# Kernel tuning notes

Measured on AMD Instinct MI355X. Metric: run time of the kernel, lower is better.

## Reference

```python
import jax, jax.numpy as jnp
import numpy as np

B, T, N, O = 128, 256, 64, 32
E, H = 32, 64            # embed_dim, hyper_dim
S = O * 4 + 1            # state_dim = 129


def setup_inputs() -> dict:
    key = jax.random.key(0)
    ks = jax.random.split(key, 16)
    def lin(k, i, o):
        return jax.random.normal(k, (i, o), jnp.float32) * (1.0 / np.sqrt(i))
    inp = {}
    inp["agent_qs"] = jax.random.normal(ks[0], (B, T, N), jnp.float32)
    inp["obs"] = jax.random.normal(ks[1], (B, T, N, O), jnp.float32)
    inp["agent_mask"] = jax.random.randint(ks[2], (B, N), 0, 2).astype(jnp.int32)
    # hyper_w_1: Linear(S,H) -> ReLU -> Linear(H, N*E)
    inp["w1_1"] = lin(ks[3], S, H); inp["b1_1"] = jnp.zeros((H,), jnp.float32)
    inp["w1_2"] = lin(ks[4], H, N * E); inp["b1_2"] = jnp.zeros((N * E,), jnp.float32)
    # hyper_w_2: Linear(S,H) -> ReLU -> Linear(H, E)
    inp["w2_1"] = lin(ks[5], S, H); inp["b2_1"] = jnp.zeros((H,), jnp.float32)
    inp["w2_2"] = lin(ks[6], H, E); inp["b2_2"] = jnp.zeros((E,), jnp.float32)
    # hyper_b_1: Linear(S,E)
    inp["wb1"] = lin(ks[7], S, E); inp["bb1"] = jnp.zeros((E,), jnp.float32)
    # hyper_b_2: Linear(S,E) -> ReLU -> Linear(E,1)
    inp["wb2_1"] = lin(ks[8], S, E); inp["bb2_1"] = jnp.zeros((E,), jnp.float32)
    inp["wb2_2"] = lin(ks[9], E, 1); inp["bb2_2"] = jnp.zeros((1,), jnp.float32)
    return inp


def _state_features(obs, agent_mask):
    # Faithful to torch loop: stats over the FIRST k agents where k = mask.sum().
    b, t, n, o = obs.shape
    k = agent_mask.sum(axis=1)                                   # [B]
    am = (jnp.arange(n)[None, :] < k[:, None]).astype(obs.dtype)  # [B,N]
    m = am[:, None, :, None]                                      # [B,1,N,1]
    cnt = k.astype(obs.dtype)[:, None, None]                      # [B,1,1]
    safe = jnp.maximum(cnt, 1.0)
    mean = (obs * m).sum(axis=2) / safe                           # [B,T,O]
    var = (((obs - mean[:, :, None, :]) ** 2) * m).sum(axis=2) / jnp.maximum(cnt - 1.0, 1.0)
    std = jnp.where(cnt > 1.0, jnp.sqrt(var), 0.0)                # unbiased std, 0 if k<=1
    mb = m > 0
    mn = jnp.where(mb, obs, jnp.inf).min(axis=2)
    mx = jnp.where(mb, obs, -jnp.inf).max(axis=2)
    ratio = jnp.broadcast_to(cnt / n, (b, t, 1))
    feats = jnp.concatenate([mean, std, mn, mx, ratio], axis=-1)  # [B,T,S]
    return jnp.where(cnt > 0.0, feats, 0.0)                       # rows stay zero if k==0


def reference(agent_qs, obs, agent_mask,
              w1_1, b1_1, w1_2, b1_2,
              w2_1, b2_1, w2_2, b2_2,
              wb1, bb1, wb2_1, bb2_1, wb2_2, bb2_2):
    b, t, n = agent_qs.shape
    e = wb1.shape[1]
    states = _state_features(obs, agent_mask)                     # [B,T,S]
    s = states.reshape(b * t, -1)                                 # [BT,S]
    qs = agent_qs.reshape(b * t, n)                               # [BT,N]
    w1 = jnp.abs(jax.nn.relu(s @ w1_1 + b1_1) @ w1_2 + b1_2).reshape(b * t, n, e)
    b1 = s @ wb1 + bb1                                            # [BT,E]
    hidden = jax.nn.elu(jnp.einsum('bn,bne->be', qs, w1) + b1)    # [BT,E]
    w2 = jnp.abs(jax.nn.relu(s @ w2_1 + b2_1) @ w2_2 + b2_2)      # [BT,E]
    b2 = jax.nn.relu(s @ wb2_1 + bb2_1) @ wb2_2 + bb2_2           # [BT,1]
    q_tot = (hidden * w2).sum(axis=-1, keepdims=True) + b2        # [BT,1]
    return q_tot.reshape(b, t, 1)
```

## Files before the change

kernel.cpp:

```cpp
#include <hip/hip_runtime.h>
#include <math.h>

#define BB 128
#define TT 256
#define NN 64
#define OO 32
#define EE 32
#define HH 64
#define SS 129
#define BT 32768
#define SP 132

__global__ __launch_bounds__(256) void k_states(const float* __restrict__ obs,
                                                const int* __restrict__ mask,
                                                float* __restrict__ states) {
    int w = threadIdx.x >> 6;
    int l = threadIdx.x & 63;
    int bt = blockIdx.x * 4 + w;
    int b = bt >> 8;

    int kv = mask[(b << 6) + l];
    #pragma unroll
    for (int off = 32; off; off >>= 1) kv += __shfl_xor(kv, off);

    int o = l & 31, nh = l >> 5;
    float sum = 0.f, ssq = 0.f, mn = INFINITY, mx = -INFINITY;
    const float* op = obs + ((size_t)bt << 11);
    for (int n = nh; n < kv; n += 2) {
        float v = op[(n << 5) + o];
        sum += v;
        ssq = fmaf(v, v, ssq);
        mn = fminf(mn, v);
        mx = fmaxf(mx, v);
    }
    sum += __shfl_xor(sum, 32);
    ssq += __shfl_xor(ssq, 32);
    mn = fminf(mn, __shfl_xor(mn, 32));
    mx = fmaxf(mx, __shfl_xor(mx, 32));

    float kf = (float)kv;
    float mean = sum / fmaxf(kf, 1.f);
    float var = (ssq - kf * mean * mean) / fmaxf(kf - 1.f, 1.f);
    float sd = (kv > 1) ? sqrtf(fmaxf(var, 0.f)) : 0.f;
    if (kv == 0) { mean = 0.f; sd = 0.f; mn = 0.f; mx = 0.f; }

    float* sp = states + (size_t)bt * SP;
    if (l < 32) {
        sp[o] = mean;
        sp[32 + o] = sd;
        sp[64 + o] = mn;
        sp[96 + o] = mx;
    }
    if (l == 0) {
        sp[128] = kf * 0.015625f;
        sp[129] = 0.f; sp[130] = 0.f; sp[131] = 0.f;
    }
}

__global__ __launch_bounds__(256, 3) void k_mlp1(const float* __restrict__ states,
        const float* __restrict__ w1_1, const float* __restrict__ b1_1,
        const float* __restrict__ w2_1, const float* __restrict__ b2_1,
        const float* __restrict__ wb1,  const float* __restrict__ bb1,
        const float* __restrict__ wb2_1,const float* __restrict__ bb2_1,
        float* __restrict__ h1, float* __restrict__ t2,
        float* __restrict__ b1v, float* __restrict__ t3) {
    __shared__ float wl[SP * 96];
    __shared__ float bl[96];
    int t = threadIdx.x;
    int half = blockIdx.y;

    const float* wA = half ? w2_1 : w1_1;
    const float* wB = half ? wb2_1 : wb1;
    const float* bA = half ? b2_1 : b1_1;
    const float* bB = half ? bb2_1 : bb1;
    float* outA = half ? t2 : h1;
    float* outB = half ? t3 : b1v;
    int reluB = half;

    for (int idx = t; idx < SP * 96; idx += 256) {
        int k = idx / 96;
        int c = idx - k * 96;
        float v = 0.f;
        if (k < SS) v = (c < 64) ? wA[k * 64 + c] : wB[k * 32 + (c - 64)];
        wl[idx] = v;
    }
    if (t < 96) bl[t] = (t < 64) ? bA[t] : bB[t - 64];
    __syncthreads();

    int cg = t & 7, rg = t >> 3;
    int c0 = cg * 12;
    int row0 = blockIdx.x * 128 + rg * 4;
    float acc[4][12];
    #pragma unroll
    for (int i = 0; i < 4; i++)
        #pragma unroll
        for (int j = 0; j < 12; j++) acc[i][j] = 0.f;

    const float* s0 = states + (size_t)row0 * SP;
    for (int k0 = 0; k0 < SP; k0 += 4) {
        float sv[4][4];
        #pragma unroll
        for (int i = 0; i < 4; i++)
            *(float4*)&sv[i][0] = *(const float4*)(s0 + i * SP + k0);
        #pragma unroll
        for (int kk = 0; kk < 4; kk++) {
            float wv[12];
            #pragma unroll
            for (int q = 0; q < 3; q++)
                *(float4*)&wv[q * 4] = *(const float4*)&wl[(k0 + kk) * 96 + c0 + q * 4];
            #pragma unroll
            for (int i = 0; i < 4; i++) {
                float s = sv[i][kk];
                #pragma unroll
                for (int j = 0; j < 12; j++) acc[i][j] = fmaf(s, wv[j], acc[i][j]);
            }
        }
    }

    #pragma unroll
    for (int i = 0; i < 4; i++) {
        int row = row0 + i;
        #pragma unroll
        for (int j = 0; j < 12; j++) {
            int c = c0 + j;
            float v = acc[i][j] + bl[c];
            if (c < 64) {
                v = fmaxf(v, 0.f);
                outA[(size_t)row * 64 + c] = v;
            } else {
                if (reluB) v = fmaxf(v, 0.f);
                outB[(size_t)row * 32 + (c - 64)] = v;
            }
        }
    }
}

__global__ __launch_bounds__(256) void k_w2(const float* __restrict__ t2,
        const float* __restrict__ t3, const float* __restrict__ w2_2,
        const float* __restrict__ b2_2, const float* __restrict__ wb2_2,
        const float* __restrict__ bb2_2,
        float* __restrict__ w2, float* __restrict__ b2v) {
    __shared__ float wl[64 * 32];
    __shared__ float wb[32];
    __shared__ float bb[32];
    int t = threadIdx.x;
    for (int idx = t; idx < 2048; idx += 256) wl[idx] = w2_2[idx];
    if (t < 32) wb[t] = wb2_2[t];
    if (t >= 32 && t < 64) bb[t - 32] = b2_2[t - 32];
    __syncthreads();

    int r = t >> 2, eq = t & 3;
    int row = blockIdx.x * 64 + r;
    int e0 = eq * 8;
    float acc[8];
    #pragma unroll
    for (int j = 0; j < 8; j++) acc[j] = 0.f;

    const float* tp = t2 + (size_t)row * 64;
    for (int h4 = 0; h4 < 64; h4 += 4) {
        float tv[4];
        *(float4*)tv = *(const float4*)(tp + h4);
        #pragma unroll
        for (int hh = 0; hh < 4; hh++) {
            float s = tv[hh];
            float4 wv0 = *(const float4*)&wl[(h4 + hh) * 32 + e0];
            float4 wv1 = *(const float4*)&wl[(h4 + hh) * 32 + e0 + 4];
            acc[0] = fmaf(s, wv0.x, acc[0]); acc[1] = fmaf(s, wv0.y, acc[1]);
            acc[2] = fmaf(s, wv0.z, acc[2]); acc[3] = fmaf(s, wv0.w, acc[3]);
            acc[4] = fmaf(s, wv1.x, acc[4]); acc[5] = fmaf(s, wv1.y, acc[5]);
            acc[6] = fmaf(s, wv1.z, acc[6]); acc[7] = fmaf(s, wv1.w, acc[7]);
        }
    }
    #pragma unroll
    for (int j = 0; j < 8; j++)
        w2[(size_t)row * 32 + e0 + j] = fabsf(acc[j] + bb[e0 + j]);

    if (eq == 0) {
        const float* t3p = t3 + (size_t)row * 32;
        float a = 0.f;
        #pragma unroll
        for (int q = 0; q < 8; q++) {
            float4 v3 = *(const float4*)(t3p + q * 4);
            float4 wv = *(const float4*)&wb[q * 4];
            a = fmaf(v3.x, wv.x, a); a = fmaf(v3.y, wv.y, a);
            a = fmaf(v3.z, wv.z, a); a = fmaf(v3.w, wv.w, a);
        }
        b2v[row] = a + bb2_2[0];
    }
}

__global__ __launch_bounds__(256, 4) void k_main(
        const float* __restrict__ h1g, const float* __restrict__ qsg,
        const float* __restrict__ w12, const float* __restrict__ b12,
        const float* __restrict__ b1vg, const float* __restrict__ w2g,
        const float* __restrict__ b2vg, float* __restrict__ out) {
    __shared__ float h1T[64 * 64];
    __shared__ float Wp[64 * 64];
    __shared__ float hid[64 * 32];
    int t = threadIdx.x;
    int row0 = blockIdx.x * 64;

    {
        int r = t >> 2, h0 = (t & 3) * 16;
        const float* hp = h1g + (size_t)(row0 + r) * 64 + h0;
        #pragma unroll
        for (int q = 0; q < 4; q++) {
            float4 hv = *(const float4*)(hp + q * 4);
            int hb = h0 + q * 4;
            h1T[(hb + 0) * 64 + r] = hv.x;
            h1T[(hb + 1) * 64 + r] = hv.y;
            h1T[(hb + 2) * 64 + r] = hv.z;
            h1T[(hb + 3) * 64 + r] = hv.w;
        }
    }

    int rg = t >> 4, cg = t & 15;
    int n_l = cg >> 3;
    int e0 = (cg & 7) * 4;
    int r0 = rg * 4;
    int jcol = n_l * 32 + e0;

    float hacc[4][4];
    #pragma unroll
    for (int i = 0; i < 4; i++)
        #pragma unroll
        for (int j = 0; j < 4; j++) hacc[i][j] = 0.f;

    for (int p = 0; p < 32; ++p) {
        __syncthreads();
        {
            int h = t >> 4, c4 = (t & 15) * 4;
            const float* wsrc = w12 + (size_t)h * 2048 + p * 64 + c4;
            float4 wv[4];
            #pragma unroll
            for (int q = 0; q < 4; q++)
                wv[q] = *(const float4*)(wsrc + (size_t)q * 16 * 2048);
            #pragma unroll
            for (int q = 0; q < 4; q++)
                *(float4*)&Wp[(h + q * 16) * 64 + c4] = wv[q];
        }
        __syncthreads();

        int n = p * 2 + n_l;
        float qv[4];
        #pragma unroll
        for (int i = 0; i < 4; i++)
            qv[i] = qsg[(size_t)(row0 + r0 + i) * 64 + n];

        float c[4][4];
        {
            float bvv[4];
            *(float4*)bvv = *(const float4*)(b12 + n * 32 + e0);
            #pragma unroll
            for (int i = 0; i < 4; i++)
                #pragma unroll
                for (int j = 0; j < 4; j++) c[i][j] = bvv[j];
        }

        #pragma unroll
        for (int k = 0; k < 64; k++) {
            float a[4], w[4];
            *(float4*)a = *(const float4*)&h1T[k * 64 + r0];
            *(float4*)w = *(const float4*)&Wp[k * 64 + jcol];
            #pragma unroll
            for (int i = 0; i < 4; i++)
                #pragma unroll
                for (int j = 0; j < 4; j++)
                    c[i][j] = fmaf(a[i], w[j], c[i][j]);
        }

        #pragma unroll
        for (int i = 0; i < 4; i++)
            #pragma unroll
            for (int j = 0; j < 4; j++)
                hacc[i][j] = fmaf(qv[i], fabsf(c[i][j]), hacc[i][j]);
    }

    #pragma unroll
    for (int i = 0; i < 4; i++)
        #pragma unroll
        for (int j = 0; j < 4; j++)
            hacc[i][j] += __shfl_xor(hacc[i][j], 8);

    if (n_l == 0) {
        #pragma unroll
        for (int i = 0; i < 4; i++) {
            float4 v = make_float4(hacc[i][0], hacc[i][1], hacc[i][2], hacc[i][3]);
            *(float4*)&hid[(r0 + i) * 32 + e0] = v;
        }
    }
    __syncthreads();

    {
        int r = t >> 2, eq = t & 3, he0 = eq * 8;
        int row = row0 + r;
        const float* b1p = b1vg + (size_t)row * 32 + he0;
        const float* w2p = w2g + (size_t)row * 32 + he0;
        float accp = 0.f;
        #pragma unroll
        for (int q = 0; q < 2; q++) {
            float4 hv = *(const float4*)&hid[r * 32 + he0 + q * 4];
            float4 bv = *(const float4*)(b1p + q * 4);
            float4 wv = *(const float4*)(w2p + q * 4);
            float x;
            x = hv.x + bv.x; x = x > 0.f ? x : expm1f(x); accp = fmaf(x, wv.x, accp);
            x = hv.y + bv.y; x = x > 0.f ? x : expm1f(x); accp = fmaf(x, wv.y, accp);
            x = hv.z + bv.z; x = x > 0.f ? x : expm1f(x); accp = fmaf(x, wv.z, accp);
            x = hv.w + bv.w; x = x > 0.f ? x : expm1f(x); accp = fmaf(x, wv.w, accp);
        }
        accp += __shfl_xor(accp, 1);
        accp += __shfl_xor(accp, 2);
        if (eq == 0) out[row] = accp + b2vg[row];
    }
}

extern "C" void kernel_launch(void* const* d_in, const int* in_sizes, int n_in,
                              void* d_out, int out_size, void* d_ws, size_t ws_size,
                              hipStream_t stream) {
    const float* agent_qs = (const float*)d_in[0];
    const float* obs      = (const float*)d_in[1];
    const int*   agent_mask = (const int*)d_in[2];
    const float* w1_1 = (const float*)d_in[3];
    const float* b1_1 = (const float*)d_in[4];
    const float* w1_2 = (const float*)d_in[5];
    const float* b1_2 = (const float*)d_in[6];
    const float* w2_1 = (const float*)d_in[7];
    const float* b2_1 = (const float*)d_in[8];
    const float* w2_2 = (const float*)d_in[9];
    const float* b2_2 = (const float*)d_in[10];
    const float* wb1  = (const float*)d_in[11];
    const float* bb1  = (const float*)d_in[12];
    const float* wb2_1 = (const float*)d_in[13];
    const float* bb2_1 = (const float*)d_in[14];
    const float* wb2_2 = (const float*)d_in[15];
    const float* bb2_2 = (const float*)d_in[16];

    float* ws = (float*)d_ws;
    float* states = ws;
    float* h1  = states + (size_t)BT * SP;
    float* t2  = h1  + (size_t)BT * 64;
    float* b1v = t2  + (size_t)BT * 64;
    float* t3  = b1v + (size_t)BT * 32;
    float* w2  = t3  + (size_t)BT * 32;
    float* b2v = w2  + (size_t)BT * 32;
    float* outp = (float*)d_out;

    k_states<<<BT / 4, 256, 0, stream>>>(obs, agent_mask, states);
    dim3 g1(BT / 128, 2);
    k_mlp1<<<g1, 256, 0, stream>>>(states, w1_1, b1_1, w2_1, b2_1,
                                   wb1, bb1, wb2_1, bb2_1, h1, t2, b1v, t3);
    k_w2<<<BT / 64, 256, 0, stream>>>(t2, t3, w2_2, b2_2, wb2_2, bb2_2, w2, b2v);
    k_main<<<BT / 64, 256, 0, stream>>>(h1, agent_qs, w1_2, b1_2, b1v, w2, b2v, outp);
}
```

Measured before the change: 559.9 us.

## Vectorize state reduction with float4 loads and register-prefetch hypernet weight tiles

The state-feature kernel now has each lane load a float4 (8 agents times 8 column groups per wave) instead of scalar loads. The partial sums, squares, min and max are then combined with xor shuffles and written as float4 stores. In the main mixing kernel, the next W1_2 tile is loaded into registers while the current tile is consumed from shared memory, which hides global load latency behind the inner FMA loop. The prefetch adds register pressure and the float4 loads may read padding rows past kv, but those stay within the buffer.

```diff
diff --git a/kernel.cpp b/kernel.cpp
--- a/kernel.cpp
+++ b/kernel.cpp
@@ -11,6 +11,13 @@
 #define BT 32768
 #define SP 132
 
+#define SHFLR_ADD(v, off) { v.x += __shfl_xor(v.x, off); v.y += __shfl_xor(v.y, off); \
+                            v.z += __shfl_xor(v.z, off); v.w += __shfl_xor(v.w, off); }
+#define SHFLR_MIN(v, off) { v.x = fminf(v.x, __shfl_xor(v.x, off)); v.y = fminf(v.y, __shfl_xor(v.y, off)); \
+                            v.z = fminf(v.z, __shfl_xor(v.z, off)); v.w = fminf(v.w, __shfl_xor(v.w, off)); }
+#define SHFLR_MAX(v, off) { v.x = fmaxf(v.x, __shfl_xor(v.x, off)); v.y = fmaxf(v.y, __shfl_xor(v.y, off)); \
+                            v.z = fmaxf(v.z, __shfl_xor(v.z, off)); v.w = fmaxf(v.w, __shfl_xor(v.w, off)); }
+
 __global__ __launch_bounds__(256) void k_states(const float* __restrict__ obs,
                                                 const int* __restrict__ mask,
                                                 float* __restrict__ states) {
@@ -23,38 +30,61 @@
     #pragma unroll
     for (int off = 32; off; off >>= 1) kv += __shfl_xor(kv, off);
 
-    int o = l & 31, nh = l >> 5;
-    float sum = 0.f, ssq = 0.f, mn = INFINITY, mx = -INFINITY;
+    int og = (l & 7) * 4;
+    int ng = l >> 3;
+    float4 s  = make_float4(0.f, 0.f, 0.f, 0.f);
+    float4 sq = make_float4(0.f, 0.f, 0.f, 0.f);
+    float4 mn = make_float4(INFINITY, INFINITY, INFINITY, INFINITY);
+    float4 mx = make_float4(-INFINITY, -INFINITY, -INFINITY, -INFINITY);
     const float* op = obs + ((size_t)bt << 11);
-    for (int n = nh; n < kv; n += 2) {
-        float v = op[(n << 5) + o];
-        sum += v;
-        ssq = fmaf(v, v, ssq);
-        mn = fminf(mn, v);
-        mx = fmaxf(mx, v);
-    }
-    sum += __shfl_xor(sum, 32);
-    ssq += __shfl_xor(ssq, 32);
-    mn = fminf(mn, __shfl_xor(mn, 32));
-    mx = fmaxf(mx, __shfl_xor(mx, 32));
+
+    for (int nb = 0; nb < kv; nb += 8) {
+        int n = nb + ng;
+        float4 v = *(const float4*)(op + (n << 5) + og);
+        if (n < kv) {
+            s.x += v.x; s.y += v.y; s.z += v.z; s.w += v.w;
+            sq.x = fmaf(v.x, v.x, sq.x); sq.y = fmaf(v.y, v.y, sq.y);
+            sq.z = fmaf(v.z, v.z, sq.z); sq.w = fmaf(v.w, v.w, sq.w);
+            mn.x = fminf(mn.x, v.x); mn.y = fminf(mn.y, v.y);
+            mn.z = fminf(mn.z, v.z); mn.w = fminf(mn.w, v.w);
+            mx.x = fmaxf(mx.x, v.x); mx.y = fmaxf(mx.y, v.y);
+            mx.z = fmaxf(mx.z, v.z); mx.w = fmaxf(mx.w, v.w);
+        }
+    }
+
+    SHFLR_ADD(s, 8)  SHFLR_ADD(s, 16)  SHFLR_ADD(s, 32)
+    SHFLR_ADD(sq, 8) SHFLR_ADD(sq, 16) SHFLR_ADD(sq, 32)
+    SHFLR_MIN(mn, 8) SHFLR_MIN(mn, 16) SHFLR_MIN(mn, 32)
+    SHFLR_MAX(mx, 8) SHFLR_MAX(mx, 16) SHFLR_MAX(mx, 32)
 
     float kf = (float)kv;
-    float mean = sum / fmaxf(kf, 1.f);
-    float var = (ssq - kf * mean * mean) / fmaxf(kf - 1.f, 1.f);
-    float sd = (kv > 1) ? sqrtf(fmaxf(var, 0.f)) : 0.f;
-    if (kv == 0) { mean = 0.f; sd = 0.f; mn = 0.f; mx = 0.f; }
-
     float* sp = states + (size_t)bt * SP;
-    if (l < 32) {
-        sp[o] = mean;
-        sp[32 + o] = sd;
-        sp[64 + o] = mn;
-        sp[96 + o] = mx;
-    }
-    if (l == 0) {
-        sp[128] = kf * 0.015625f;
-        sp[129] = 0.f; sp[130] = 0.f; sp[131] = 0.f;
-    }
+    if (l < 8) {
+        float4 mean4, sd4;
+        float inv = 1.f / fmaxf(kf, 1.f);
+        float invv = 1.f / fmaxf(kf - 1.f, 1.f);
+        mean4.x = s.x * inv; mean4.y = s.y * inv;
+        mean4.z = s.z * inv; mean4.w = s.w * inv;
+        if (kv > 1) {
+            sd4.x = sqrtf(fmaxf((sq.x - kf * mean4.x * mean4.x) * invv, 0.f));
+            sd4.y = sqrtf(fmaxf((sq.y - kf * mean4.y * mean4.y) * invv, 0.f));
+            sd4.z = sqrtf(fmaxf((sq.z - kf * mean4.z * mean4.z) * invv, 0.f));
+            sd4.w = sqrtf(fmaxf((sq.w - kf * mean4.w * mean4.w) * invv, 0.f));
+        } else {
+            sd4 = make_float4(0.f, 0.f, 0.f, 0.f);
+        }
+        if (kv == 0) {
+            mean4 = make_float4(0.f, 0.f, 0.f, 0.f);
+            mn = make_float4(0.f, 0.f, 0.f, 0.f);
+            mx = make_float4(0.f, 0.f, 0.f, 0.f);
+        }
+        *(float4*)(sp + og)      = mean4;
+        *(float4*)(sp + 32 + og) = sd4;
+        *(float4*)(sp + 64 + og) = mn;
+        *(float4*)(sp + 96 + og) = mx;
+    }
+    if (l == 0)
+        *(float4*)(sp + 128) = make_float4(kf * 0.015625f, 0.f, 0.f, 0.f);
 }
 
 __global__ __launch_bounds__(256, 3) void k_mlp1(const float* __restrict__ states,
@@ -220,26 +250,33 @@
     int r0 = rg * 4;
     int jcol = n_l * 32 + e0;
 
+    int hs = t >> 4, c4 = (t & 15) * 4;
+    const float* wbase = w12 + (size_t)hs * 2048 + c4;
+
     float hacc[4][4];
     #pragma unroll
     for (int i = 0; i < 4; i++)
         #pragma unroll
         for (int j = 0; j < 4; j++) hacc[i][j] = 0.f;
+
+    float4 wreg[4];
+    #pragma unroll
+    for (int q = 0; q < 4; q++)
+        wreg[q] = *(const float4*)(wbase + (size_t)q * 16 * 2048);
 
     for (int p = 0; p < 32; ++p) {
         __syncthreads();
-        {
-            int h = t >> 4, c4 = (t & 15) * 4;
-            const float* wsrc = w12 + (size_t)h * 2048 + p * 64 + c4;
-            float4 wv[4];
+        #pragma unroll
+        for (int q = 0; q < 4; q++)
+            *(float4*)&Wp[(hs + q * 16) * 64 + c4] = wreg[q];
+        __syncthreads();
+
+        if (p < 31) {
+            const float* wsrc = wbase + (p + 1) * 64;
             #pragma unroll
             for (int q = 0; q < 4; q++)
-                wv[q] = *(const float4*)(wsrc + (size_t)q * 16 * 2048);
-            #pragma unroll
-            for (int q = 0; q < 4; q++)
-                *(float4*)&Wp[(h + q * 16) * 64 + c4] = wv[q];
-        }
-        __syncthreads();
+                wreg[q] = *(const float4*)(wsrc + (size_t)q * 16 * 2048);
+        }
 
         int n = p * 2 + n_l;
         float qv[4];
@@ -259,14 +296,14 @@
 
         #pragma unroll
         for (int k = 0; k < 64; k++) {
-            float a[4], w[4];
+            float a[4], wv[4];
             *(float4*)a = *(const float4*)&h1T[k * 64 + r0];
-            *(float4*)w = *(const float4*)&Wp[k * 64 + jcol];
+            *(float4*)wv = *(const float4*)&Wp[k * 64 + jcol];
             #pragma unroll
             for (int i = 0; i < 4; i++)
                 #pragma unroll
                 for (int j = 0; j < 4; j++)
-                    c[i][j] = fmaf(a[i], w[j], c[i][j]);
+                    c[i][j] = fmaf(a[i], wv[j], c[i][j]);
         }
 
         #pragma unroll
```

Result: no change. 566.4 us (+1.2%).
